# Kernel optimization log

Measured on AMD Instinct MI355X. Metric: run time of the kernel, lower is better.

The kernel has to match this reference:

```python
import jax, jax.numpy as jnp
import numpy as np

E = 131072   # total messages
N = 8192     # dim_size (num nodes)
D = 256      # input_dim == hidden_dim (forced by h + m add)


def setup_inputs() -> dict:
    key = jax.random.key(0)
    k1, k2, k3, k4, k5 = jax.random.split(key, 5)
    msg = jax.random.normal(k1, (E, D), dtype=jnp.float32)
    index = jax.random.randint(k2, (E,), 0, N)
    t = jax.random.uniform(k3, (E,), dtype=jnp.float32)
    # torch.nn.Linear(D, D) params (kaiming-uniform-ish scale)
    W = jax.random.normal(k4, (D, D), dtype=jnp.float32) / np.sqrt(D)
    b = (jax.random.normal(k5, (D,), dtype=jnp.float32) * 0.01)
    return {"msg": msg, "index": index, "t": t, "dim_size": N, "W": W, "b": b}


def reference(msg, index, t, dim_size, W, b):
    # Original: for each node, sort its messages by t, then run the linear
    # recurrence h <- W @ (m + h) + b starting from h = 0; nodes with no
    # messages keep h = 0. Vectorized: one global stable sort by (index, t),
    # then a single segmented lax.scan with reset at segment boundaries.
    num_msgs, d = msg.shape
    order = jnp.lexsort((t, index))          # primary key: index, secondary: t
    m_sorted = msg[order]                     # [E, d]
    seg = index[order]                        # [E]

    def step(carry, inp):
        h, prev = carry
        m, s = inp
        h_in = jnp.where(s == prev, h, jnp.zeros_like(h))  # reset at new segment
        h_new = (m + h_in) @ W.T + b
        return (h_new, s), h_new

    init = (jnp.zeros((d,), msg.dtype), jnp.asarray(-1, seg.dtype))
    _, ys = jax.lax.scan(step, init, (m_sorted, seg))      # ys: [E, d]

    # final hidden per node = h at the last message of its segment
    pos = jnp.arange(num_msgs)
    last = jax.ops.segment_max(pos, seg, num_segments=dim_size)
    counts = jax.ops.segment_sum(jnp.ones((num_msgs,), jnp.int32), seg,
                                 num_segments=dim_size)
    gathered = ys[jnp.clip(last, 0, num_msgs - 1)]          # [N, d]
    hidden = jnp.where((counts > 0)[:, None], gathered, jnp.zeros_like(gathered))
    return hidden
```

## Files before the change

### kernel.cpp

```cpp
#include <hip/hip_runtime.h>
#include <hip/hip_bf16.h>

#define E_MSGS 131072
#define N_NODES 8192
#define D_DIM 256
#define XA_STRIDE 264

typedef __bf16 bf16x8 __attribute__((ext_vector_type(8)));
typedef float f32x4 __attribute__((ext_vector_type(4)));


__global__ void k_zero(int* counts, int* cursors) {
    int i = blockIdx.x * blockDim.x + threadIdx.x;
    if (i < N_NODES) { counts[i] = 0; cursors[i] = 0; }
}

__global__ void k_count(const int* __restrict__ index, int* __restrict__ counts) {
    int e = blockIdx.x * blockDim.x + threadIdx.x;
    if (e < E_MSGS) atomicAdd(&counts[index[e]], 1);
}

__global__ void k_scan(const int* __restrict__ counts, int* __restrict__ offsets) {
    __shared__ int partial[256];
    int tid = threadIdx.x;
    int base = tid * 32;
    int local[32];
    int sum = 0;
#pragma unroll
    for (int i = 0; i < 32; i++) { local[i] = sum; sum += counts[base + i]; }
    partial[tid] = sum;
    __syncthreads();
    for (int off = 1; off < 256; off <<= 1) {
        int v = (tid >= off) ? partial[tid - off] : 0;
        __syncthreads();
        partial[tid] += v;
        __syncthreads();
    }
    int basesum = (tid > 0) ? partial[tid - 1] : 0;
#pragma unroll
    for (int i = 0; i < 32; i++) offsets[base + i] = basesum + local[i];
    if (tid == 255) offsets[N_NODES] = partial[255];
}

__global__ void k_scatter(const int* __restrict__ index, const int* __restrict__ offsets,
                          int* __restrict__ cursors, int* __restrict__ bucket) {
    int e = blockIdx.x * blockDim.x + threadIdx.x;
    if (e < E_MSGS) {
        int n = index[e];
        int p = offsets[n] + atomicAdd(&cursors[n], 1);
        bucket[p] = e;
    }
}

__global__ void k_rank(const int* __restrict__ index, const float* __restrict__ t,
                       const int* __restrict__ offsets, const int* __restrict__ bucket,
                       int* __restrict__ sorted_id) {
    int p = blockIdx.x * blockDim.x + threadIdx.x;
    if (p < E_MSGS) {
        int e = bucket[p];
        int n = index[e];
        int beg = offsets[n], end = offsets[n + 1];
        float te = t[e];
        int r = 0;
        for (int q = beg; q < end; q++) {
            int e2 = bucket[q];
            float t2 = t[e2];
            r += (t2 < te) || (t2 == te && e2 < e);
        }
        sorted_id[beg + r] = e;
    }
}


__launch_bounds__(256, 2)
__global__ void k_gru(const float* __restrict__ msg, const float* __restrict__ W,
                      const float* __restrict__ b, const int* __restrict__ offsets,
                      const int* __restrict__ sorted_id, float* __restrict__ out) {
    __shared__ __bf16 xA[2][16 * XA_STRIDE];

    int tid  = threadIdx.x;
    int wave = tid >> 6;
    int lane = tid & 63;
    int q    = lane >> 4;
    int l    = lane & 15;
    int node0 = blockIdx.x * 16;

    bf16x8 wf[8][4];
#pragma unroll
    for (int t4 = 0; t4 < 4; t4++) {
        const float* wr = W + (64 * wave + 16 * t4 + l) * D_DIM;
#pragma unroll
        for (int c = 0; c < 8; c++) {
            int k0 = 32 * c + 8 * q;
            float4 w0 = *(const float4*)(wr + k0);
            float4 w1 = *(const float4*)(wr + k0 + 4);
            bf16x8 f;
            f[0] = (__bf16)w0.x; f[1] = (__bf16)w0.y; f[2] = (__bf16)w0.z; f[3] = (__bf16)w0.w;
            f[4] = (__bf16)w1.x; f[5] = (__bf16)w1.y; f[6] = (__bf16)w1.z; f[7] = (__bf16)w1.w;
            wf[c][t4] = f;
        }
    }
    float bias[4];
#pragma unroll
    for (int t4 = 0; t4 < 4; t4++) bias[t4] = b[64 * wave + 16 * t4 + l];

    int off4[4], cnt4[4];
#pragma unroll
    for (int r = 0; r < 4; r++) {
        int node = node0 + 4 * q + r;
        int o0 = offsets[node], o1 = offsets[node + 1];
        off4[r] = o0; cnt4[r] = o1 - o0;
    }
    int S = 0;
    for (int i = 0; i < 16; i++) {
        int c = offsets[node0 + i + 1] - offsets[node0 + i];
        S = max(S, c);
    }

    float h[4][4];
#pragma unroll
    for (int t4 = 0; t4 < 4; t4++)
#pragma unroll
        for (int r = 0; r < 4; r++) h[t4][r] = 0.f;

#pragma unroll
    for (int r = 0; r < 4; r++) {
        float mv[4];
        if (0 < cnt4[r]) {
            int sid = sorted_id[off4[r]];
            const float* mrow = msg + (long)sid * D_DIM;
#pragma unroll
            for (int t4 = 0; t4 < 4; t4++) mv[t4] = mrow[64 * wave + 16 * t4 + l];
        } else {
#pragma unroll
            for (int t4 = 0; t4 < 4; t4++) mv[t4] = 0.f;
        }
#pragma unroll
        for (int t4 = 0; t4 < 4; t4++)
            xA[0][(4 * q + r) * XA_STRIDE + 64 * wave + 16 * t4 + l] = (__bf16)mv[t4];
    }
    __syncthreads();

    for (int s = 0; s < S; s++) {
        const __bf16* buf = xA[s & 1];
        f32x4 acc[4];
#pragma unroll
        for (int t4 = 0; t4 < 4; t4++) acc[t4] = (f32x4){0.f, 0.f, 0.f, 0.f};
#pragma unroll
        for (int c = 0; c < 8; c++) {
            bf16x8 a = *(const bf16x8*)(buf + l * XA_STRIDE + 32 * c + 8 * q);
#pragma unroll
            for (int t4 = 0; t4 < 4; t4++)
                acc[t4] = __builtin_amdgcn_mfma_f32_16x16x32_bf16(a, wf[c][t4], acc[t4], 0, 0, 0);
        }

        float mv[4][4];
#pragma unroll
        for (int r = 0; r < 4; r++) {
            if (s + 1 < cnt4[r]) {
                int sid = sorted_id[off4[r] + s + 1];
                const float* mrow = msg + (long)sid * D_DIM;
#pragma unroll
                for (int t4 = 0; t4 < 4; t4++) mv[r][t4] = mrow[64 * wave + 16 * t4 + l];
            } else {
#pragma unroll
                for (int t4 = 0; t4 < 4; t4++) mv[r][t4] = 0.f;
            }
        }

        __bf16* nbuf = xA[(s + 1) & 1];
#pragma unroll
        for (int t4 = 0; t4 < 4; t4++) {
#pragma unroll
            for (int r = 0; r < 4; r++) {
                float hn = acc[t4][r] + bias[t4];
                bool valid = s < cnt4[r];
                h[t4][r] = valid ? hn : h[t4][r];
                nbuf[(4 * q + r) * XA_STRIDE + 64 * wave + 16 * t4 + l] =
                    (__bf16)(h[t4][r] + mv[r][t4]);
            }
        }
        __syncthreads();
    }

#pragma unroll
    for (int t4 = 0; t4 < 4; t4++)
#pragma unroll
        for (int r = 0; r < 4; r++)
            out[(long)(node0 + 4 * q + r) * D_DIM + 64 * wave + 16 * t4 + l] = h[t4][r];
}


extern "C" void kernel_launch(void* const* d_in, const int* in_sizes, int n_in,
                              void* d_out, int out_size, void* d_ws, size_t ws_size,
                              hipStream_t stream) {
    const float* msg   = (const float*)d_in[0];
    const int*   index = (const int*)d_in[1];
    const float* t     = (const float*)d_in[2];
    const float* W     = (const float*)d_in[4];
    const float* b     = (const float*)d_in[5];
    float* out = (float*)d_out;

    int* ws = (int*)d_ws;
    int* counts    = ws;
    int* offsets   = ws + 8192;
    int* cursors   = ws + 24576;
    int* bucket    = ws + 32768;
    int* sorted_id = ws + 163840;

    k_zero<<<N_NODES / 256, 256, 0, stream>>>(counts, cursors);
    k_count<<<E_MSGS / 256, 256, 0, stream>>>(index, counts);
    k_scan<<<1, 256, 0, stream>>>(counts, offsets);
    k_scatter<<<E_MSGS / 256, 256, 0, stream>>>(index, offsets, cursors, bucket);
    k_rank<<<E_MSGS / 256, 256, 0, stream>>>(index, t, offsets, bucket, sorted_id);
    k_gru<<<N_NODES / 16, 256, 0, stream>>>(msg, W, b, offsets, sorted_id, out);
}
```

Measured before the change: 304.4 us.

## Sort nodes by message count and prefetch messages into LDS asynchronously

Builds a permutation of nodes ordered by message count (descending histogram bucket sort inside the scan kernel), so that each 16-node block in the recurrence kernel holds nodes with similar segment lengths, reducing wasted steps bounded by the block maximum. Message rows are prefetched two steps ahead with global_load_lds into a double-buffered LDS staging area instead of synchronous per-step global loads. The zeroing kernel is replaced with a memset. This adds LDS usage, which may lower occupancy, and adds serial work in the single-block prep kernel.

```diff
diff --git a/kernel.cpp b/kernel.cpp
--- a/kernel.cpp
+++ b/kernel.cpp
@@ -9,25 +9,35 @@
 typedef __bf16 bf16x8 __attribute__((ext_vector_type(8)));
 typedef float f32x4 __attribute__((ext_vector_type(4)));
 
-
-__global__ void k_zero(int* counts, int* cursors) {
-    int i = blockIdx.x * blockDim.x + threadIdx.x;
-    if (i < N_NODES) { counts[i] = 0; cursors[i] = 0; }
-}
+typedef const __attribute__((address_space(1))) void cg_void;
+typedef __attribute__((address_space(3))) void lds_void;
+
 
 __global__ void k_count(const int* __restrict__ index, int* __restrict__ counts) {
     int e = blockIdx.x * blockDim.x + threadIdx.x;
     if (e < E_MSGS) atomicAdd(&counts[index[e]], 1);
 }
 
-__global__ void k_scan(const int* __restrict__ counts, int* __restrict__ offsets) {
+__global__ void k_prep(const int* __restrict__ counts, int* __restrict__ offsets,
+                       int* __restrict__ perm) {
     __shared__ int partial[256];
+    __shared__ int hist[256];
+    __shared__ int hscan[256];
+    __shared__ int hcur[256];
     int tid = threadIdx.x;
+    hist[tid] = 0;
+    __syncthreads();
+
     int base = tid * 32;
     int local[32];
     int sum = 0;
 #pragma unroll
-    for (int i = 0; i < 32; i++) { local[i] = sum; sum += counts[base + i]; }
+    for (int i = 0; i < 32; i++) {
+        local[i] = sum;
+        int c = counts[base + i];
+        sum += c;
+        atomicAdd(&hist[min(c, 255)], 1);
+    }
     partial[tid] = sum;
     __syncthreads();
     for (int off = 1; off < 256; off <<= 1) {
@@ -40,6 +50,24 @@
 #pragma unroll
     for (int i = 0; i < 32; i++) offsets[base + i] = basesum + local[i];
     if (tid == 255) offsets[N_NODES] = partial[255];
+
+    hscan[tid] = hist[255 - tid];
+    __syncthreads();
+    for (int off = 1; off < 256; off <<= 1) {
+        int v = (tid >= off) ? hscan[tid - off] : 0;
+        __syncthreads();
+        hscan[tid] += v;
+        __syncthreads();
+    }
+    hcur[tid] = hscan[255 - tid] - hist[tid];
+    __syncthreads();
+#pragma unroll
+    for (int i = 0; i < 32; i++) {
+        int n = base + i;
+        int c = min(counts[n], 255);
+        int pos = atomicAdd(&hcur[c], 1);
+        perm[pos] = n;
+    }
 }
 
 __global__ void k_scatter(const int* __restrict__ index, const int* __restrict__ offsets,
@@ -75,8 +103,10 @@
 __launch_bounds__(256, 2)
 __global__ void k_gru(const float* __restrict__ msg, const float* __restrict__ W,
                       const float* __restrict__ b, const int* __restrict__ offsets,
-                      const int* __restrict__ sorted_id, float* __restrict__ out) {
+                      const int* __restrict__ sorted_id, const int* __restrict__ perm,
+                      float* __restrict__ out) {
     __shared__ __bf16 xA[2][16 * XA_STRIDE];
+    __shared__ float msg_lds[2][16][D_DIM];
 
     int tid  = threadIdx.x;
     int wave = tid >> 6;
@@ -104,17 +134,48 @@
 #pragma unroll
     for (int t4 = 0; t4 < 4; t4++) bias[t4] = b[64 * wave + 16 * t4 + l];
 
-    int off4[4], cnt4[4];
+    int nodeC[4], off4[4], cnt4[4];
 #pragma unroll
     for (int r = 0; r < 4; r++) {
-        int node = node0 + 4 * q + r;
-        int o0 = offsets[node], o1 = offsets[node + 1];
+        int n = perm[node0 + 4 * q + r];
+        nodeC[r] = n;
+        int o0 = offsets[n], o1 = offsets[n + 1];
         off4[r] = o0; cnt4[r] = o1 - o0;
     }
     int S = 0;
     for (int i = 0; i < 16; i++) {
-        int c = offsets[node0 + i + 1] - offsets[node0 + i];
-        S = max(S, c);
+        int n = perm[node0 + i];
+        S = max(S, offsets[n + 1] - offsets[n]);
+    }
+
+    int offG[4];
+#pragma unroll
+    for (int j = 0; j < 4; j++) offG[j] = offsets[perm[node0 + 4 * wave + j]];
+
+#pragma unroll
+    for (int j = 0; j < 4; j++) {
+        int sid0 = sorted_id[min(offG[j], E_MSGS - 1)];
+        int sid1 = sorted_id[min(offG[j] + 1, E_MSGS - 1)];
+        const float* g0 = msg + (long)sid0 * D_DIM + 4 * lane;
+        const float* g1 = msg + (long)sid1 * D_DIM + 4 * lane;
+        float* l0 = &msg_lds[0][4 * wave + j][4 * lane];
+        float* l1 = &msg_lds[1][4 * wave + j][4 * lane];
+        __builtin_amdgcn_global_load_lds((cg_void*)g0, (lds_void*)l0, 16, 0, 0);
+        __builtin_amdgcn_global_load_lds((cg_void*)g1, (lds_void*)l1, 16, 0, 0);
+    }
+    int sidg[4];
+#pragma unroll
+    for (int j = 0; j < 4; j++) sidg[j] = sorted_id[min(offG[j] + 2, E_MSGS - 1)];
+    __syncthreads();
+
+    {
+        int row = tid >> 4;
+        int c0  = tid & 15;
+#pragma unroll
+        for (int k = 0; k < 16; k++) {
+            int col = c0 + 16 * k;
+            xA[0][row * XA_STRIDE + col] = (__bf16)msg_lds[0][row][col];
+        }
     }
 
     float h[4][4];
@@ -122,26 +183,19 @@
     for (int t4 = 0; t4 < 4; t4++)
 #pragma unroll
         for (int r = 0; r < 4; r++) h[t4][r] = 0.f;
-
-#pragma unroll
-    for (int r = 0; r < 4; r++) {
-        float mv[4];
-        if (0 < cnt4[r]) {
-            int sid = sorted_id[off4[r]];
-            const float* mrow = msg + (long)sid * D_DIM;
-#pragma unroll
-            for (int t4 = 0; t4 < 4; t4++) mv[t4] = mrow[64 * wave + 16 * t4 + l];
-        } else {
-#pragma unroll
-            for (int t4 = 0; t4 < 4; t4++) mv[t4] = 0.f;
-        }
-#pragma unroll
-        for (int t4 = 0; t4 < 4; t4++)
-            xA[0][(4 * q + r) * XA_STRIDE + 64 * wave + 16 * t4 + l] = (__bf16)mv[t4];
-    }
     __syncthreads();
 
     for (int s = 0; s < S; s++) {
+#pragma unroll
+        for (int j = 0; j < 4; j++) {
+            const float* g = msg + (long)sidg[j] * D_DIM + 4 * lane;
+            float* ld = &msg_lds[s & 1][4 * wave + j][4 * lane];
+            __builtin_amdgcn_global_load_lds((cg_void*)g, (lds_void*)ld, 16, 0, 0);
+        }
+#pragma unroll
+        for (int j = 0; j < 4; j++)
+            sidg[j] = sorted_id[min(offG[j] + s + 3, E_MSGS - 1)];
+
         const __bf16* buf = xA[s & 1];
         f32x4 acc[4];
 #pragma unroll
@@ -154,21 +208,8 @@
                 acc[t4] = __builtin_amdgcn_mfma_f32_16x16x32_bf16(a, wf[c][t4], acc[t4], 0, 0, 0);
         }
 
-        float mv[4][4];
-#pragma unroll
-        for (int r = 0; r < 4; r++) {
-            if (s + 1 < cnt4[r]) {
-                int sid = sorted_id[off4[r] + s + 1];
-                const float* mrow = msg + (long)sid * D_DIM;
-#pragma unroll
-                for (int t4 = 0; t4 < 4; t4++) mv[r][t4] = mrow[64 * wave + 16 * t4 + l];
-            } else {
-#pragma unroll
-                for (int t4 = 0; t4 < 4; t4++) mv[r][t4] = 0.f;
-            }
-        }
-
         __bf16* nbuf = xA[(s + 1) & 1];
+        const float (*mbuf)[D_DIM] = msg_lds[(s + 1) & 1];
 #pragma unroll
         for (int t4 = 0; t4 < 4; t4++) {
 #pragma unroll
@@ -176,8 +217,9 @@
                 float hn = acc[t4][r] + bias[t4];
                 bool valid = s < cnt4[r];
                 h[t4][r] = valid ? hn : h[t4][r];
+                float mv = mbuf[4 * q + r][64 * wave + 16 * t4 + l];
                 nbuf[(4 * q + r) * XA_STRIDE + 64 * wave + 16 * t4 + l] =
-                    (__bf16)(h[t4][r] + mv[r][t4]);
+                    (__bf16)(h[t4][r] + mv);
             }
         }
         __syncthreads();
@@ -187,7 +229,7 @@
     for (int t4 = 0; t4 < 4; t4++)
 #pragma unroll
         for (int r = 0; r < 4; r++)
-            out[(long)(node0 + 4 * q + r) * D_DIM + 64 * wave + 16 * t4 + l] = h[t4][r];
+            out[(long)nodeC[r] * D_DIM + 64 * wave + 16 * t4 + l] = h[t4][r];
 }
 
 
@@ -203,15 +245,16 @@
 
     int* ws = (int*)d_ws;
     int* counts    = ws;
-    int* offsets   = ws + 8192;
-    int* cursors   = ws + 24576;
-    int* bucket    = ws + 32768;
-    int* sorted_id = ws + 163840;
-
-    k_zero<<<N_NODES / 256, 256, 0, stream>>>(counts, cursors);
+    int* cursors   = ws + 8192;
+    int* offsets   = ws + 16384;
+    int* perm      = ws + 24584;
+    int* bucket    = ws + 32776;
+    int* sorted_id = ws + 163848;
+
+    hipMemsetAsync(counts, 0, 16384 * sizeof(int), stream);
     k_count<<<E_MSGS / 256, 256, 0, stream>>>(index, counts);
-    k_scan<<<1, 256, 0, stream>>>(counts, offsets);
+    k_prep<<<1, 256, 0, stream>>>(counts, offsets, perm);
     k_scatter<<<E_MSGS / 256, 256, 0, stream>>>(index, offsets, cursors, bucket);
     k_rank<<<E_MSGS / 256, 256, 0, stream>>>(index, t, offsets, bucket, sorted_id);
-    k_gru<<<N_NODES / 16, 256, 0, stream>>>(msg, W, b, offsets, sorted_id, out);
-}
+    k_gru<<<N_NODES / 16, 256, 0, stream>>>(msg, W, b, offsets, sorted_id, perm, out);
+}
```

Result: faster. 262.4 us (-13.8%).
